# Optimization experiments

Hardware: AMD Instinct MI355X
Metric: run time of the kernel (lower is better)

## Reference

```python
import jax, jax.numpy as jnp
import numpy as np

B, S, D, H, L = 128, 256, 128, 4, 2
N = S - 1            # tree nodes (complete binary tree, depths 0..7)
MAX_DEPTH = 7
NEG = -1e9
EPS = 1e-6


def _binary_tree_topology():
    n = np.arange(N)
    parent = np.where(n > 0, (n - 1) // 2, 0).astype(np.int32)   # parent(0) dummy
    depth = np.floor(np.log2(n + 1)).astype(np.int32)            # BFS level
    is_leaf = (2 * n + 1 >= N)
    return parent, depth, is_leaf


def setup_inputs() -> dict:
    key = jax.random.key(0)
    ks = jax.random.split(key, 6)
    p_np, d_np, l_np = _binary_tree_topology()
    parent = jnp.broadcast_to(jnp.asarray(p_np), (B, N))
    depth = jnp.broadcast_to(jnp.asarray(d_np), (B, N))
    is_leaf = jnp.broadcast_to(jnp.asarray(l_np), (B, N))
    x = jax.random.normal(ks[0], (B, S, D), jnp.float32)
    mask = jnp.zeros((B, 1, 1, S), jnp.float32)  # full trees -> no padding
    sc = 1.0 / np.sqrt(D)
    Wq = jax.random.normal(ks[1], (L, D, D), jnp.float32) * sc
    Wk = jax.random.normal(ks[2], (L, D, D), jnp.float32) * sc
    Wv = jax.random.normal(ks[3], (L, D, D), jnp.float32) * sc
    Wo = jax.random.normal(ks[4], (L, D, D), jnp.float32) * sc
    bq = jnp.zeros((L, D)); bk = jnp.zeros((L, D)); bv = jnp.zeros((L, D)); bo = jnp.zeros((L, D))
    g1 = jnp.ones((L, D)); b1 = jnp.zeros((L, D))
    g2 = jnp.ones((L, D)); b2 = jnp.zeros((L, D))
    return dict(x=x, mask=mask, parent=parent, depth=depth, is_leaf=is_leaf,
                Wq=Wq, bq=bq, Wk=Wk, bk=bk, Wv=Wv, bv=bv, Wo=Wo, bo=bo,
                g1=g1, b1=b1, g2=g2, b2=b2)


def _layernorm(x, g, b):
    mu = jnp.mean(x, axis=-1, keepdims=True)
    var = jnp.mean(jnp.square(x - mu), axis=-1, keepdims=True)
    return g * (x - mu) * jax.lax.rsqrt(var + EPS) + b


def _tree_agg(x, parent, depth, is_leaf):
    """Vectorized bottom-up tree aggregation (agg='sum': tanh(sum children)).
    Seq positions map to tree nodes in BFS order; last position passes through."""
    e = x[:, :N]                                            # [B, N, D]
    seg = (parent + (jnp.arange(B) * N)[:, None]).reshape(-1)  # flat parent ids
    for d in range(MAX_DEPTH, 0, -1):                       # deepest level -> root
        contrib = jnp.where((depth == d)[..., None], e, 0.0)
        agg = jax.ops.segment_sum(contrib.reshape(B * N, D), seg,
                                  num_segments=B * N).reshape(B, N, D)
        upd = ((depth == d - 1) & (~is_leaf))[..., None]    # internal nodes at d-1
        e = jnp.where(upd, jnp.tanh(agg), e)
    return jnp.concatenate([e, x[:, N:]], axis=1)


def reference(x, mask, parent, depth, is_leaf,
              Wq, bq, Wk, bk, Wv, bv, Wo, bo, g1, b1, g2, b2):
    Dh = D // H
    scale = 1.0 / jnp.sqrt(jnp.float32(Dh))
    losses = []
    weights = None
    for l in range(L):
        q = (jnp.einsum('bsd,de->bse', x, Wq[l]) + bq[l]).reshape(B, S, H, Dh).transpose(0, 2, 1, 3)
        k = (jnp.einsum('bsd,de->bse', x, Wk[l]) + bk[l]).reshape(B, S, H, Dh).transpose(0, 2, 1, 3)
        v = (jnp.einsum('bsd,de->bse', x, Wv[l]) + bv[l]).reshape(B, S, H, Dh).transpose(0, 2, 1, 3)
        logits = jnp.einsum('bhqd,bhkd->bhqk', q, k) * scale + mask * NEG
        attn = jax.nn.softmax(logits, axis=-1)              # [B, H, S, S]
        ctx = jnp.einsum('bhqk,bhkd->bhqd', attn, v).transpose(0, 2, 1, 3).reshape(B, S, D)
        att_out = jnp.einsum('bsd,de->bse', ctx, Wo[l]) + bo[l]
        out1 = _layernorm(x + att_out, g1[l], b1[l])
        tab = _tree_agg(out1, parent, depth, is_leaf)       # dropout: eval -> identity
        x = _layernorm(out1 + tab, g2[l], b2[l])
        weights = attn[:, :, -1, :]
        losses.append(jnp.sum(jnp.abs(weights)))
    total_l1 = jnp.sum(jnp.stack(losses))
    return x, total_l1, weights
```

## Files before the change

kernel.cpp:

```cpp
#include <hip/hip_runtime.h>
#include <math.h>

typedef __bf16 bf16x8 __attribute__((ext_vector_type(8)));
typedef __bf16 bf16x4 __attribute__((ext_vector_type(4)));
typedef __bf16 bf16x2 __attribute__((ext_vector_type(2)));
typedef float f32x4 __attribute__((ext_vector_type(4)));

namespace {
constexpr int kB = 128, kS = 256, kD = 128, kH = 4;
constexpr float kEps = 1e-6f;
constexpr float kScale = 0.17677669529663687f;
constexpr float kNeg = -1000000000.0f;
constexpr float kLog2e = 1.4426950408889634f;
constexpr size_t kSZ = (size_t)kB * kS * kD;
}

__device__ __forceinline__ void glds16(const void* g, void* l) {
    __builtin_amdgcn_global_load_lds(
        (const __attribute__((address_space(1))) unsigned int*)g,
        (__attribute__((address_space(3))) unsigned int*)l, 16, 0, 0);
}

__global__ __launch_bounds__(256) void wtrans(
    const float* __restrict__ Wq, const float* __restrict__ Wk,
    const float* __restrict__ Wv, const float* __restrict__ Wo,
    __bf16* __restrict__ Wt)
{
    const int mtx = blockIdx.x & 3, l = blockIdx.x >> 2;
    const float* W = (mtx == 0 ? Wq : mtx == 1 ? Wk : mtx == 2 ? Wv : Wo) +
                     (size_t)l * kD * kD;
    __bf16* o = Wt + (size_t)blockIdx.x * kD * kD;
    for (int idx = threadIdx.x; idx < kD * kD; idx += 256) {
        const int k = idx >> 7, n = idx & 127;
        const int lo = n & 15, ni = n >> 4;
        const int j = k & 7, tt = k >> 3, g = tt & 3, ks = tt >> 2;
        o[((ni * 4 + ks) * 64 + g * 16 + lo) * 8 + j] = (__bf16)W[idx];
    }
}

template <int WEIGHTS, bool F32X>
__global__ __launch_bounds__(512) void mega_attn(
    const void* __restrict__ xsrc, const __bf16* __restrict__ Wp,
    const float* __restrict__ bq, const float* __restrict__ bk,
    const float* __restrict__ bv, const float* __restrict__ bo,
    const float* __restrict__ mask, const float* __restrict__ gamma,
    const float* __restrict__ beta, __bf16* __restrict__ O1,
    float* __restrict__ wout, float* __restrict__ l1out)
{
    __shared__ __bf16 Xs[256 * 128];
    __shared__ __bf16 Kls[256 * 32];
    __shared__ __bf16 Vt[32][276];
    __shared__ __bf16 Pl[8][16 * 64];
    __shared__ __bf16 Qs[8][16 * 32];
    __shared__ __bf16 Ctx[128 * 128];
    __shared__ float mb[256];

    const int t = threadIdx.x;
    const int w = t >> 6, l = t & 63, lo = l & 15, g = l >> 4;
    const int b = blockIdx.x & 127, strip = blockIdx.x >> 7;
    const int q0 = strip * 128 + w * 16;
    const int tk0 = w * 32;
    const int kswz = (lo ^ (lo >> 2)) & 3;

    const __bf16* Wqp = Wp;
    const __bf16* Wkp = Wp + 16384;
    const __bf16* Wvp = Wp + 2 * 16384;
    const __bf16* Wop = Wp + 3 * 16384;

    if constexpr (F32X) {
#pragma unroll
        for (int p = 0; p < 8; ++p) {
            const int ci = p * 512 + t;
            const int row = ci >> 4, c = ci & 15;
            const float* src = (const float*)xsrc +
                               ((size_t)b * 256 + row) * 128 + c * 8;
            const float4 a0 = *(const float4*)src;
            const float4 a1 = *(const float4*)(src + 4);
            bf16x8 o;
            o[0] = (__bf16)a0.x; o[1] = (__bf16)a0.y; o[2] = (__bf16)a0.z; o[3] = (__bf16)a0.w;
            o[4] = (__bf16)a1.x; o[5] = (__bf16)a1.y; o[6] = (__bf16)a1.z; o[7] = (__bf16)a1.w;
            *(bf16x8*)&Xs[row * 128 + ((c ^ (row & 7)) << 3)] = o;
        }
    } else {
#pragma unroll
        for (int it = 0; it < 8; ++it)
            glds16((const __bf16*)xsrc + (size_t)b * 32768 + (it * 8 + w) * 512 + l * 8,
                   &Xs[(it * 8 + w) * 512]);
    }
    if (t < 256) mb[t] = mask[b * 256 + t] * (kNeg * kLog2e);
    if (WEIGHTS && blockIdx.x == 0 && t == 0) l1out[0] = 1024.0f;
    __syncthreads();

    auto wfrag = [&](const __bf16* W, int ni, int ks) {
        return *(const bf16x8*)(W + (((ni * 4 + ks) * 64 + l) << 3));
    };
    auto xfrag = [&](int row, int ks) {
        return *(const bf16x8*)&Xs[row * 128 + (((g + 4 * ks) ^ (row & 7)) << 3)];
    };

    bf16x8 xa[2][4], xq[4];
#pragma unroll
    for (int ks = 0; ks < 4; ++ks) {
        xa[0][ks] = xfrag(tk0 + lo, ks);
        xa[1][ks] = xfrag(tk0 + 16 + lo, ks);
        xq[ks] = xfrag(q0 + lo, ks);
    }

    f32x4 kacc[2][2], vacc[2][2], qacc[2];

    auto produce_compute = [&](int h) {
#pragma unroll
        for (int i = 0; i < 2; ++i)
#pragma unroll
            for (int j2 = 0; j2 < 2; ++j2) {
                kacc[i][j2] = f32x4{0.f, 0.f, 0.f, 0.f};
                vacc[i][j2] = f32x4{0.f, 0.f, 0.f, 0.f};
            }
        qacc[0] = f32x4{0.f, 0.f, 0.f, 0.f};
        qacc[1] = f32x4{0.f, 0.f, 0.f, 0.f};
#pragma unroll
        for (int ks = 0; ks < 4; ++ks) {
            const bf16x8 wk0 = wfrag(Wkp, 2 * h, ks);
            const bf16x8 wk1 = wfrag(Wkp, 2 * h + 1, ks);
            const bf16x8 wv0 = wfrag(Wvp, 2 * h, ks);
            const bf16x8 wv1 = wfrag(Wvp, 2 * h + 1, ks);
            kacc[0][0] = __builtin_amdgcn_mfma_f32_16x16x32_bf16(wk0, xa[0][ks], kacc[0][0], 0, 0, 0);
            kacc[0][1] = __builtin_amdgcn_mfma_f32_16x16x32_bf16(wk0, xa[1][ks], kacc[0][1], 0, 0, 0);
            kacc[1][0] = __builtin_amdgcn_mfma_f32_16x16x32_bf16(wk1, xa[0][ks], kacc[1][0], 0, 0, 0);
            kacc[1][1] = __builtin_amdgcn_mfma_f32_16x16x32_bf16(wk1, xa[1][ks], kacc[1][1], 0, 0, 0);
            vacc[0][0] = __builtin_amdgcn_mfma_f32_16x16x32_bf16(xa[0][ks], wv0, vacc[0][0], 0, 0, 0);
            vacc[1][0] = __builtin_amdgcn_mfma_f32_16x16x32_bf16(xa[1][ks], wv0, vacc[1][0], 0, 0, 0);
            vacc[0][1] = __builtin_amdgcn_mfma_f32_16x16x32_bf16(xa[0][ks], wv1, vacc[0][1], 0, 0, 0);
            vacc[1][1] = __builtin_amdgcn_mfma_f32_16x16x32_bf16(xa[1][ks], wv1, vacc[1][1], 0, 0, 0);
            qacc[0] = __builtin_amdgcn_mfma_f32_16x16x32_bf16(xq[ks], wfrag(Wqp, 2 * h, ks), qacc[0], 0, 0, 0);
            qacc[1] = __builtin_amdgcn_mfma_f32_16x16x32_bf16(xq[ks], wfrag(Wqp, 2 * h + 1, ks), qacc[1], 0, 0, 0);
        }
    };

    auto produce_write = [&](int h) {
#pragma unroll
        for (int dm = 0; dm < 2; ++dm) {
            const f32x4 bkv = *(const f32x4*)(bk + h * 32 + dm * 16 + 4 * g);
            const int pos = ((dm * 2 + (g >> 1)) ^ kswz) << 3;
            const int sub = (4 * g) & 7;
#pragma unroll
            for (int tj = 0; tj < 2; ++tj) {
                bf16x4 kv;
#pragma unroll
                for (int r = 0; r < 4; ++r) kv[r] = (__bf16)(kacc[dm][tj][r] + bkv[r]);
                const int key = tk0 + tj * 16 + lo;
                *(bf16x4*)&Kls[key * 32 + pos + sub] = kv;
            }
        }
#pragma unroll
        for (int nj = 0; nj < 2; ++nj) {
            const float bvv = bv[h * 32 + nj * 16 + lo];
#pragma unroll
            for (int mi = 0; mi < 2; ++mi) {
                bf16x4 vv4;
#pragma unroll
                for (int r = 0; r < 4; ++r) vv4[r] = (__bf16)(vacc[mi][nj][r] + bvv);
                *(bf16x4*)&Vt[nj * 16 + lo][tk0 + mi * 16 + 4 * g] = vv4;
            }
        }
#pragma unroll
        for (int nj = 0; nj < 2; ++nj) {
            const float bqv = bq[h * 32 + nj * 16 + lo];
#pragma unroll
            for (int r = 0; r < 4; ++r)
                Qs[w][(4 * g + r) * 32 + nj * 16 + lo] = (__bf16)(qacc[nj][r] + bqv);
        }
    };

    produce_compute(0);
    produce_write(0);
    __syncthreads();

#pragma unroll
    for (int h = 0; h < 4; ++h) {
        const bf16x8 qf = *(const bf16x8*)&Qs[w][lo * 32 + g * 8];
        f32x4 s[16];
        __builtin_amdgcn_s_setprio(1);
#pragma unroll
        for (int f = 0; f < 16; ++f) {
            const bf16x8 kf =
                *(const bf16x8*)&Kls[(f * 16 + lo) * 32 + ((g ^ kswz) << 3)];
            s[f] = __builtin_amdgcn_mfma_f32_16x16x32_bf16(
                kf, qf, f32x4{0.f, 0.f, 0.f, 0.f}, 0, 0, 0);
        }
        __builtin_amdgcn_s_setprio(0);

        float ls = 0.f;
#pragma unroll
        for (int f = 0; f < 16; ++f) {
            const f32x4 mk = *(const f32x4*)&mb[f * 16 + g * 4];
#pragma unroll
            for (int r = 0; r < 4; ++r) {
                const float p = __builtin_amdgcn_exp2f(
                    s[f][r] * (kScale * kLog2e) + mk[r]);
                s[f][r] = p;
                ls += p;
            }
        }
        ls += __shfl_xor(ls, 16, 64);
        ls += __shfl_xor(ls, 32, 64);

        if constexpr (WEIGHTS) {
            if (strip == 1 && w == 7 && lo == 15) {
                const float inv = 1.f / ls;
                float* wrow = wout + ((size_t)b * 4 + h) * 256;
#pragma unroll
                for (int f = 0; f < 16; ++f)
#pragma unroll
                    for (int r = 0; r < 4; ++r)
                        wrow[f * 16 + g * 4 + r] = s[f][r] * inv;
            }
        }

        f32x4 o[2] = {f32x4{0.f, 0.f, 0.f, 0.f}, f32x4{0.f, 0.f, 0.f, 0.f}};
#pragma unroll
        for (int qt = 0; qt < 4; ++qt) {
#pragma unroll
            for (int fl = 0; fl < 4; ++fl) {
                const int ff = qt * 4 + fl;
#pragma unroll
                for (int pr = 0; pr < 2; ++pr) {
                    bf16x2 pk;
                    pk[0] = (__bf16)s[ff][2 * pr];
                    pk[1] = (__bf16)s[ff][2 * pr + 1];
                    const int e = fl * 16 + 4 * g + 2 * pr;
                    const int addr =
                        lo * 64 + ((((e >> 3) ^ (lo & 7)) << 3) | (e & 7));
                    *(bf16x2*)&Pl[w][addr] = pk;
                }
            }
            __builtin_amdgcn_s_setprio(1);
#pragma unroll
            for (int ksl = 0; ksl < 2; ++ksl) {
                const int cc = ksl * 4 + g;
                const bf16x8 pa =
                    *(const bf16x8*)&Pl[w][lo * 64 + ((cc ^ (lo & 7)) << 3)];
#pragma unroll
                for (int nf = 0; nf < 2; ++nf) {
                    const bf16x8 bvv =
                        *(const bf16x8*)&Vt[nf * 16 + lo][(qt * 2 + ksl) * 32 + g * 8];
                    o[nf] = __builtin_amdgcn_mfma_f32_16x16x32_bf16(pa, bvv, o[nf], 0, 0, 0);
                }
            }
            __builtin_amdgcn_s_setprio(0);
        }

        if (h < 3) produce_compute(h + 1);

#pragma unroll
        for (int r = 0; r < 4; ++r) {
            const float inv = 1.f / __shfl(ls, 4 * g + r, 64);
            const int crow = w * 16 + g * 4 + r;
#pragma unroll
            for (int nf = 0; nf < 2; ++nf) {
                const int col = h * 32 + nf * 16 + lo;
                const int chunk = (col >> 3) ^ (crow & 7);
                Ctx[crow * 128 + (chunk << 3) + (col & 7)] = (__bf16)(o[nf][r] * inv);
            }
        }
        if (h < 3) {
            __syncthreads();
            produce_write(h + 1);
            __syncthreads();
        }
    }

    const size_t m0 = (size_t)b * 256 + strip * 128;
    f32x4 acc[8];
#pragma unroll
    for (int ni = 0; ni < 8; ++ni) acc[ni] = f32x4{0.f, 0.f, 0.f, 0.f};

    const int arow = w * 16 + lo;
#pragma unroll
    for (int ks = 0; ks < 4; ++ks) {
        const bf16x8 av =
            *(const bf16x8*)&Ctx[arow * 128 + (((g + 4 * ks) ^ (arow & 7)) << 3)];
#pragma unroll
        for (int ni = 0; ni < 8; ++ni)
            acc[ni] = __builtin_amdgcn_mfma_f32_16x16x32_bf16(
                av, wfrag(Wop, ni, ks), acc[ni], 0, 0, 0);
    }

    float bcol[8], ga[8], be[8];
#pragma unroll
    for (int ni = 0; ni < 8; ++ni) {
        bcol[ni] = bo[ni * 16 + lo];
        ga[ni] = gamma[ni * 16 + lo];
        be[ni] = beta[ni * 16 + lo];
    }

    float vv[4][8];
    float s[4] = {0, 0, 0, 0}, s2[4] = {0, 0, 0, 0};
#pragma unroll
    for (int r = 0; r < 4; ++r) {
        const int local = strip * 128 + w * 16 + g * 4 + r;
#pragma unroll
        for (int ni = 0; ni < 8; ++ni) {
            const int col = ni * 16 + lo;
            const int chunk = (col >> 3) ^ (local & 7);
            const float rv = (float)Xs[local * 128 + (chunk << 3) + (col & 7)];
            const float x = acc[ni][r] + bcol[ni] + rv;
            vv[r][ni] = x; s[r] += x; s2[r] += x * x;
        }
    }
#pragma unroll
    for (int r = 0; r < 4; ++r)
#pragma unroll
        for (int o = 1; o < 16; o <<= 1) {
            s[r] += __shfl_xor(s[r], o, 64);
            s2[r] += __shfl_xor(s2[r], o, 64);
        }
#pragma unroll
    for (int r = 0; r < 4; ++r) {
        const float mu = s[r] * (1.f / 128.f);
        const float var = s2[r] * (1.f / 128.f) - mu * mu;
        const float rs = rsqrtf(var + kEps);
        const size_t mm = m0 + w * 16 + g * 4 + r;
#pragma unroll
        for (int ni = 0; ni < 8; ++ni)
            O1[mm * 128 + ni * 16 + lo] =
                (__bf16)(ga[ni] * (vv[r][ni] - mu) * rs + be[ni]);
    }
}

__global__ __launch_bounds__(1024) void tree_ln(
    const __bf16* __restrict__ o1, const float* __restrict__ gamma,
    const float* __restrict__ beta, float* __restrict__ xo,
    __bf16* __restrict__ xb, int wf32, int wbf16)
{
    __shared__ float e[127 * 132];
    const int isleaf = blockIdx.x >> 7;
    const int b = blockIdx.x & 127;
    const int t = threadIdx.x;
    const __bf16* ob = o1 + (size_t)b * 256 * 128;
    const int wv = t >> 6, lane = t & 63;
    const float2 gv = *(const float2*)(gamma + lane * 2);
    const float2 bb = *(const float2*)(beta + lane * 2);
    const int c = lane * 2;

    auto ln_store = [&](int row, float y0, float y1) {
        float s = y0 + y1, s2 = y0 * y0 + y1 * y1;
#pragma unroll
        for (int o = 1; o < 64; o <<= 1) {
            s += __shfl_xor(s, o, 64);
            s2 += __shfl_xor(s2, o, 64);
        }
        const float mu = s * (1.f / 128.f);
        const float var = s2 * (1.f / 128.f) - mu * mu;
        const float rs = rsqrtf(var + kEps);
        const float r0 = gv.x * (y0 - mu) * rs + bb.x;
        const float r1 = gv.y * (y1 - mu) * rs + bb.y;
        const size_t rowoff = ((size_t)b * 256 + row) * 128;
        if (wf32) {
            float2 o2; o2.x = r0; o2.y = r1;
            *(float2*)(xo + rowoff + c) = o2;
        }
        if (wbf16) {
            const int chunk = (c >> 3) ^ (row & 7);
            bf16x2 ob2; ob2[0] = (__bf16)r0; ob2[1] = (__bf16)r1;
            *(bf16x2*)(xb + rowoff + chunk * 8 + (c & 7)) = ob2;
        }
    };

    if (isleaf) {
        for (int row = 128 + wv; row < 256; row += 16) {
            const bf16x2 v = *(const bf16x2*)(ob + (size_t)row * 128 + c);
            ln_store(row, 2.f * (float)v[0], 2.f * (float)v[1]);
        }
        return;
    }

    {
        const int p = 63 + (t >> 4);
        const int cg = (t & 15) * 8;
        const bf16x8 c1 = *(const bf16x8*)(ob + (size_t)(2 * p + 1) * 128 + cg);
        const bf16x8 c2 = *(const bf16x8*)(ob + (size_t)(2 * p + 2) * 128 + cg);
        f32x4 r0, r1;
#pragma unroll
        for (int i = 0; i < 4; ++i)
            r0[i] = tanhf((float)c1[i] + (float)c2[i]);
#pragma unroll
        for (int i = 0; i < 4; ++i)
            r1[i] = tanhf((float)c1[4 + i] + (float)c2[4 + i]);
        *(f32x4*)&e[p * 132 + cg] = r0;
        *(f32x4*)&e[p * 132 + cg + 4] = r1;
    }
    __syncthreads();

    {
        const int col = wv * 8 + (lane & 7);
        const int nsub = lane >> 3;
        for (int lvl = 5; lvl >= 0; --lvl) {
            const int p0 = (1 << lvl) - 1;
            const int cnt = 1 << lvl;
            for (int base = 0; base < cnt; base += 8) {
                const int p = p0 + base + nsub;
                if (base + nsub < cnt) {
                    e[p * 132 + col] =
                        tanhf(e[(2 * p + 1) * 132 + col] + e[(2 * p + 2) * 132 + col]);
                }
            }
        }
    }
    __syncthreads();

    for (int row = wv; row < 128; row += 16) {
        const bf16x2 v = *(const bf16x2*)(ob + (size_t)row * 128 + c);
        float y0, y1;
        if (row < 127) {
            y0 = (float)v[0] + e[row * 132 + c];
            y1 = (float)v[1] + e[row * 132 + c + 1];
        } else {
            y0 = 2.f * (float)v[0];
            y1 = 2.f * (float)v[1];
        }
        ln_store(row, y0, y1);
    }
}

extern "C" void kernel_launch(void* const* d_in, const int* in_sizes, int n_in,
                              void* d_out, int out_size, void* d_ws, size_t ws_size,
                              hipStream_t stream)
{
    (void)in_sizes; (void)n_in; (void)out_size; (void)ws_size;

    const float* x_in = (const float*)d_in[0];
    const float* mask = (const float*)d_in[1];
    const float* Wq = (const float*)d_in[5];
    const float* bq = (const float*)d_in[6];
    const float* Wk = (const float*)d_in[7];
    const float* bk = (const float*)d_in[8];
    const float* Wv = (const float*)d_in[9];
    const float* bv = (const float*)d_in[10];
    const float* Wo = (const float*)d_in[11];
    const float* bo = (const float*)d_in[12];
    const float* g1 = (const float*)d_in[13];
    const float* b1 = (const float*)d_in[14];
    const float* g2 = (const float*)d_in[15];
    const float* b2 = (const float*)d_in[16];

    float* out_x = (float*)d_out;
    float* out_l1 = out_x + kSZ;
    float* out_w = out_l1 + 1;

    char* wsb = (char*)d_ws;
    __bf16* O1 = (__bf16*)wsb;
    __bf16* xb = (__bf16*)(wsb + kSZ * 2);
    __bf16* Wt = (__bf16*)(wsb + 2 * kSZ * 2);

    wtrans<<<8, 256, 0, stream>>>(Wq, Wk, Wv, Wo, Wt);

    mega_attn<0, true><<<256, 512, 0, stream>>>(x_in, Wt, bq, bk, bv, bo,
                                                mask, g1, b1, O1,
                                                nullptr, nullptr);
    tree_ln<<<256, 1024, 0, stream>>>(O1, g2, b2, nullptr, xb, 0, 1);

    mega_attn<1, false><<<256, 512, 0, stream>>>(xb, Wt + 4 * 16384,
                                                 bq + kD, bk + kD, bv + kD, bo + kD,
                                                 mask, g1 + kD, b1 + kD, O1,
                                                 out_w, out_l1);
    tree_ln<<<256, 1024, 0, stream>>>(O1, g2 + kD, b2 + kD, out_x, nullptr, 1, 0);
}
```

Measured before the change: 95.01 us.

## Fuse all layers into one persistent kernel with software grid barriers

Replaces the five separate launches (weight transpose, two attention kernels, two tree/LayerNorm kernels) with a single 256-block persistent kernel that uses atomic-counter grid barriers between phases. The leaf-row LayerNorm is folded into the attention epilogue of strip 1, so the tree phase only runs on strip-0 blocks and is remapped to 512 threads. The aim is to remove kernel launch gaps and a redundant pass over leaf rows. In exchange it needs all 256 blocks co-resident to avoid deadlock, adds a memset plus spin-wait barriers, and leaves half the blocks idle during the tree phases.

```diff
diff --git a/kernel.cpp b/kernel.cpp
--- a/kernel.cpp
+++ b/kernel.cpp
@@ -7,13 +7,23 @@
 typedef float f32x4 __attribute__((ext_vector_type(4)));
 
 namespace {
-constexpr int kB = 128, kS = 256, kD = 128, kH = 4;
+constexpr int kD = 128;
 constexpr float kEps = 1e-6f;
 constexpr float kScale = 0.17677669529663687f;
 constexpr float kNeg = -1000000000.0f;
 constexpr float kLog2e = 1.4426950408889634f;
-constexpr size_t kSZ = (size_t)kB * kS * kD;
-}
+constexpr size_t kSZ = (size_t)128 * 256 * 128;
+}
+
+struct SMem {
+    __bf16 Xs[256 * 128];
+    __bf16 Kls[256 * 32];
+    __bf16 Vt[32][276];
+    __bf16 Pl[8][1024];
+    __bf16 Qs[8][512];
+    __bf16 Ctx[128 * 128];
+    float mb[256];
+};
 
 __device__ __forceinline__ void glds16(const void* g, void* l) {
     __builtin_amdgcn_global_load_lds(
@@ -21,40 +31,26 @@
         (__attribute__((address_space(3))) unsigned int*)l, 16, 0, 0);
 }
 
-__global__ __launch_bounds__(256) void wtrans(
-    const float* __restrict__ Wq, const float* __restrict__ Wk,
-    const float* __restrict__ Wv, const float* __restrict__ Wo,
-    __bf16* __restrict__ Wt)
+__device__ __forceinline__ void gridbar(int* cnt, int nblk) {
+    __syncthreads();
+    if (threadIdx.x == 0) {
+        __threadfence();
+        atomicAdd(cnt, 1);
+        while (__hip_atomic_load(cnt, __ATOMIC_ACQUIRE,
+                                 __HIP_MEMORY_SCOPE_AGENT) < nblk)
+            __builtin_amdgcn_s_sleep(2);
+        __threadfence();
+    }
+    __syncthreads();
+}
+
+template <int WEIGHTS, bool STAGE, int LEAF2>
+__device__ void mega_phase(
+    SMem& sm, const void* xsrc, const __bf16* Wp,
+    const float* bq, const float* bk, const float* bv, const float* bo,
+    const float* g1, const float* b1, const float* g2, const float* b2,
+    __bf16* O1, float* wout, float* l1out, float* xo2, __bf16* xb2)
 {
-    const int mtx = blockIdx.x & 3, l = blockIdx.x >> 2;
-    const float* W = (mtx == 0 ? Wq : mtx == 1 ? Wk : mtx == 2 ? Wv : Wo) +
-                     (size_t)l * kD * kD;
-    __bf16* o = Wt + (size_t)blockIdx.x * kD * kD;
-    for (int idx = threadIdx.x; idx < kD * kD; idx += 256) {
-        const int k = idx >> 7, n = idx & 127;
-        const int lo = n & 15, ni = n >> 4;
-        const int j = k & 7, tt = k >> 3, g = tt & 3, ks = tt >> 2;
-        o[((ni * 4 + ks) * 64 + g * 16 + lo) * 8 + j] = (__bf16)W[idx];
-    }
-}
-
-template <int WEIGHTS, bool F32X>
-__global__ __launch_bounds__(512) void mega_attn(
-    const void* __restrict__ xsrc, const __bf16* __restrict__ Wp,
-    const float* __restrict__ bq, const float* __restrict__ bk,
-    const float* __restrict__ bv, const float* __restrict__ bo,
-    const float* __restrict__ mask, const float* __restrict__ gamma,
-    const float* __restrict__ beta, __bf16* __restrict__ O1,
-    float* __restrict__ wout, float* __restrict__ l1out)
-{
-    __shared__ __bf16 Xs[256 * 128];
-    __shared__ __bf16 Kls[256 * 32];
-    __shared__ __bf16 Vt[32][276];
-    __shared__ __bf16 Pl[8][16 * 64];
-    __shared__ __bf16 Qs[8][16 * 32];
-    __shared__ __bf16 Ctx[128 * 128];
-    __shared__ float mb[256];
-
     const int t = threadIdx.x;
     const int w = t >> 6, l = t & 63, lo = l & 15, g = l >> 4;
     const int b = blockIdx.x & 127, strip = blockIdx.x >> 7;
@@ -67,35 +63,20 @@
     const __bf16* Wvp = Wp + 2 * 16384;
     const __bf16* Wop = Wp + 3 * 16384;
 
-    if constexpr (F32X) {
-#pragma unroll
-        for (int p = 0; p < 8; ++p) {
-            const int ci = p * 512 + t;
-            const int row = ci >> 4, c = ci & 15;
-            const float* src = (const float*)xsrc +
-                               ((size_t)b * 256 + row) * 128 + c * 8;
-            const float4 a0 = *(const float4*)src;
-            const float4 a1 = *(const float4*)(src + 4);
-            bf16x8 o;
-            o[0] = (__bf16)a0.x; o[1] = (__bf16)a0.y; o[2] = (__bf16)a0.z; o[3] = (__bf16)a0.w;
-            o[4] = (__bf16)a1.x; o[5] = (__bf16)a1.y; o[6] = (__bf16)a1.z; o[7] = (__bf16)a1.w;
-            *(bf16x8*)&Xs[row * 128 + ((c ^ (row & 7)) << 3)] = o;
-        }
-    } else {
+    if constexpr (STAGE) {
 #pragma unroll
         for (int it = 0; it < 8; ++it)
             glds16((const __bf16*)xsrc + (size_t)b * 32768 + (it * 8 + w) * 512 + l * 8,
-                   &Xs[(it * 8 + w) * 512]);
-    }
-    if (t < 256) mb[t] = mask[b * 256 + t] * (kNeg * kLog2e);
+                   &sm.Xs[(it * 8 + w) * 512]);
+        __syncthreads();
+    }
     if (WEIGHTS && blockIdx.x == 0 && t == 0) l1out[0] = 1024.0f;
-    __syncthreads();
 
     auto wfrag = [&](const __bf16* W, int ni, int ks) {
         return *(const bf16x8*)(W + (((ni * 4 + ks) * 64 + l) << 3));
     };
     auto xfrag = [&](int row, int ks) {
-        return *(const bf16x8*)&Xs[row * 128 + (((g + 4 * ks) ^ (row & 7)) << 3)];
+        return *(const bf16x8*)&sm.Xs[row * 128 + (((g + 4 * ks) ^ (row & 7)) << 3)];
     };
 
     bf16x8 xa[2][4], xq[4];
@@ -149,7 +130,7 @@
 #pragma unroll
                 for (int r = 0; r < 4; ++r) kv[r] = (__bf16)(kacc[dm][tj][r] + bkv[r]);
                 const int key = tk0 + tj * 16 + lo;
-                *(bf16x4*)&Kls[key * 32 + pos + sub] = kv;
+                *(bf16x4*)&sm.Kls[key * 32 + pos + sub] = kv;
             }
         }
 #pragma unroll
@@ -160,7 +141,7 @@
                 bf16x4 vv4;
 #pragma unroll
                 for (int r = 0; r < 4; ++r) vv4[r] = (__bf16)(vacc[mi][nj][r] + bvv);
-                *(bf16x4*)&Vt[nj * 16 + lo][tk0 + mi * 16 + 4 * g] = vv4;
+                *(bf16x4*)&sm.Vt[nj * 16 + lo][tk0 + mi * 16 + 4 * g] = vv4;
             }
         }
 #pragma unroll
@@ -168,7 +149,7 @@
             const float bqv = bq[h * 32 + nj * 16 + lo];
 #pragma unroll
             for (int r = 0; r < 4; ++r)
-                Qs[w][(4 * g + r) * 32 + nj * 16 + lo] = (__bf16)(qacc[nj][r] + bqv);
+                sm.Qs[w][(4 * g + r) * 32 + nj * 16 + lo] = (__bf16)(qacc[nj][r] + bqv);
         }
     };
 
@@ -178,13 +159,13 @@
 
 #pragma unroll
     for (int h = 0; h < 4; ++h) {
-        const bf16x8 qf = *(const bf16x8*)&Qs[w][lo * 32 + g * 8];
+        const bf16x8 qf = *(const bf16x8*)&sm.Qs[w][lo * 32 + g * 8];
         f32x4 s[16];
         __builtin_amdgcn_s_setprio(1);
 #pragma unroll
         for (int f = 0; f < 16; ++f) {
             const bf16x8 kf =
-                *(const bf16x8*)&Kls[(f * 16 + lo) * 32 + ((g ^ kswz) << 3)];
+                *(const bf16x8*)&sm.Kls[(f * 16 + lo) * 32 + ((g ^ kswz) << 3)];
             s[f] = __builtin_amdgcn_mfma_f32_16x16x32_bf16(
                 kf, qf, f32x4{0.f, 0.f, 0.f, 0.f}, 0, 0, 0);
         }
@@ -193,7 +174,7 @@
         float ls = 0.f;
 #pragma unroll
         for (int f = 0; f < 16; ++f) {
-            const f32x4 mk = *(const f32x4*)&mb[f * 16 + g * 4];
+            const f32x4 mk = *(const f32x4*)&sm.mb[f * 16 + g * 4];
 #pragma unroll
             for (int r = 0; r < 4; ++r) {
                 const float p = __builtin_amdgcn_exp2f(
@@ -231,7 +212,7 @@
                     const int e = fl * 16 + 4 * g + 2 * pr;
                     const int addr =
                         lo * 64 + ((((e >> 3) ^ (lo & 7)) << 3) | (e & 7));
-                    *(bf16x2*)&Pl[w][addr] = pk;
+                    *(bf16x2*)&sm.Pl[w][addr] = pk;
                 }
             }
             __builtin_amdgcn_s_setprio(1);
@@ -239,11 +220,11 @@
             for (int ksl = 0; ksl < 2; ++ksl) {
                 const int cc = ksl * 4 + g;
                 const bf16x8 pa =
-                    *(const bf16x8*)&Pl[w][lo * 64 + ((cc ^ (lo & 7)) << 3)];
+                    *(const bf16x8*)&sm.Pl[w][lo * 64 + ((cc ^ (lo & 7)) << 3)];
 #pragma unroll
                 for (int nf = 0; nf < 2; ++nf) {
                     const bf16x8 bvv =
-                        *(const bf16x8*)&Vt[nf * 16 + lo][(qt * 2 + ksl) * 32 + g * 8];
+                        *(const bf16x8*)&sm.Vt[nf * 16 + lo][(qt * 2 + ksl) * 32 + g * 8];
                     o[nf] = __builtin_amdgcn_mfma_f32_16x16x32_bf16(pa, bvv, o[nf], 0, 0, 0);
                 }
             }
@@ -260,7 +241,7 @@
             for (int nf = 0; nf < 2; ++nf) {
                 const int col = h * 32 + nf * 16 + lo;
                 const int chunk = (col >> 3) ^ (crow & 7);
-                Ctx[crow * 128 + (chunk << 3) + (col & 7)] = (__bf16)(o[nf][r] * inv);
+                sm.Ctx[crow * 128 + (chunk << 3) + (col & 7)] = (__bf16)(o[nf][r] * inv);
             }
         }
         if (h < 3) {
@@ -279,19 +260,26 @@
 #pragma unroll
     for (int ks = 0; ks < 4; ++ks) {
         const bf16x8 av =
-            *(const bf16x8*)&Ctx[arow * 128 + (((g + 4 * ks) ^ (arow & 7)) << 3)];
+            *(const bf16x8*)&sm.Ctx[arow * 128 + (((g + 4 * ks) ^ (arow & 7)) << 3)];
 #pragma unroll
         for (int ni = 0; ni < 8; ++ni)
             acc[ni] = __builtin_amdgcn_mfma_f32_16x16x32_bf16(
                 av, wfrag(Wop, ni, ks), acc[ni], 0, 0, 0);
     }
 
-    float bcol[8], ga[8], be[8];
+    float bcol[8], ga[8], be[8], g2a[8], b2a[8];
 #pragma unroll
     for (int ni = 0; ni < 8; ++ni) {
         bcol[ni] = bo[ni * 16 + lo];
-        ga[ni] = gamma[ni * 16 + lo];
-        be[ni] = beta[ni * 16 + lo];
+        ga[ni] = g1[ni * 16 + lo];
+        be[ni] = b1[ni * 16 + lo];
+    }
+    if (LEAF2 && strip == 1) {
+#pragma unroll
+        for (int ni = 0; ni < 8; ++ni) {
+            g2a[ni] = g2[ni * 16 + lo];
+            b2a[ni] = b2[ni * 16 + lo];
+        }
     }
 
     float vv[4][8];
@@ -303,7 +291,7 @@
         for (int ni = 0; ni < 8; ++ni) {
             const int col = ni * 16 + lo;
             const int chunk = (col >> 3) ^ (local & 7);
-            const float rv = (float)Xs[local * 128 + (chunk << 3) + (col & 7)];
+            const float rv = (float)sm.Xs[local * 128 + (chunk << 3) + (col & 7)];
             const float x = acc[ni][r] + bcol[ni] + rv;
             vv[r][ni] = x; s[r] += x; s2[r] += x * x;
         }
@@ -321,29 +309,96 @@
         const float var = s2[r] * (1.f / 128.f) - mu * mu;
         const float rs = rsqrtf(var + kEps);
         const size_t mm = m0 + w * 16 + g * 4 + r;
-#pragma unroll
-        for (int ni = 0; ni < 8; ++ni)
-            O1[mm * 128 + ni * 16 + lo] =
-                (__bf16)(ga[ni] * (vv[r][ni] - mu) * rs + be[ni]);
-    }
-}
-
-__global__ __launch_bounds__(1024) void tree_ln(
-    const __bf16* __restrict__ o1, const float* __restrict__ gamma,
-    const float* __restrict__ beta, float* __restrict__ xo,
-    __bf16* __restrict__ xb, int wf32, int wbf16)
+        float yv[8];
+        float ys = 0.f, ys2 = 0.f;
+#pragma unroll
+        for (int ni = 0; ni < 8; ++ni) {
+            const __bf16 ov = (__bf16)(ga[ni] * (vv[r][ni] - mu) * rs + be[ni]);
+            O1[mm * 128 + ni * 16 + lo] = ov;
+            if (LEAF2 && strip == 1) {
+                const float y = 2.f * (float)ov;
+                yv[ni] = y; ys += y; ys2 += y * y;
+            }
+        }
+        if (LEAF2 && strip == 1) {
+#pragma unroll
+            for (int o = 1; o < 16; o <<= 1) {
+                ys += __shfl_xor(ys, o, 64);
+                ys2 += __shfl_xor(ys2, o, 64);
+            }
+            const float mu2 = ys * (1.f / 128.f);
+            const float var2 = ys2 * (1.f / 128.f) - mu2 * mu2;
+            const float rs2 = rsqrtf(var2 + kEps);
+#pragma unroll
+            for (int ni = 0; ni < 8; ++ni) {
+                const float val = g2a[ni] * (yv[ni] - mu2) * rs2 + b2a[ni];
+                const int col = ni * 16 + lo;
+                if constexpr (LEAF2 == 1) {
+                    const int chunk = (col >> 3) ^ ((int)mm & 7);
+                    xb2[mm * 128 + chunk * 8 + (col & 7)] = (__bf16)val;
+                } else if constexpr (LEAF2 == 2) {
+                    xo2[mm * 128 + col] = val;
+                }
+            }
+        }
+    }
+}
+
+__device__ void tree_phase0(
+    SMem& sm, const __bf16* O1, const float* gamma, const float* beta,
+    float* xo, __bf16* xb, int wf32, int wbf16, int b)
 {
-    __shared__ float e[127 * 132];
-    const int isleaf = blockIdx.x >> 7;
-    const int b = blockIdx.x & 127;
+    float* e = (float*)sm.Xs;
     const int t = threadIdx.x;
-    const __bf16* ob = o1 + (size_t)b * 256 * 128;
     const int wv = t >> 6, lane = t & 63;
+    const __bf16* ob = O1 + (size_t)b * 32768;
     const float2 gv = *(const float2*)(gamma + lane * 2);
     const float2 bb = *(const float2*)(beta + lane * 2);
     const int c = lane * 2;
 
-    auto ln_store = [&](int row, float y0, float y1) {
+#pragma unroll
+    for (int it = 0; it < 2; ++it) {
+        const int q = it * 512 + t;
+        const int p = 63 + (q >> 4);
+        const int cg = (q & 15) * 8;
+        const bf16x8 c1 = *(const bf16x8*)(ob + (size_t)(2 * p + 1) * 128 + cg);
+        const bf16x8 c2 = *(const bf16x8*)(ob + (size_t)(2 * p + 2) * 128 + cg);
+        f32x4 r0, r1;
+#pragma unroll
+        for (int i = 0; i < 4; ++i) r0[i] = tanhf((float)c1[i] + (float)c2[i]);
+#pragma unroll
+        for (int i = 0; i < 4; ++i) r1[i] = tanhf((float)c1[4 + i] + (float)c2[4 + i]);
+        *(f32x4*)&e[p * 128 + cg] = r0;
+        *(f32x4*)&e[p * 128 + cg + 4] = r1;
+    }
+    __syncthreads();
+
+    {
+        const int col = wv * 16 + (lane & 15);
+        const int nsub = lane >> 4;
+        for (int lvl = 5; lvl >= 0; --lvl) {
+            const int p0 = (1 << lvl) - 1;
+            const int cntn = 1 << lvl;
+            for (int base = 0; base < cntn; base += 4) {
+                const int p = p0 + base + nsub;
+                if (base + nsub < cntn)
+                    e[p * 128 + col] =
+                        tanhf(e[(2 * p + 1) * 128 + col] + e[(2 * p + 2) * 128 + col]);
+            }
+        }
+    }
+    __syncthreads();
+
+    for (int row = wv; row < 128; row += 8) {
+        const bf16x2 v = *(const bf16x2*)(ob + (size_t)row * 128 + c);
+        float y0, y1;
+        if (row < 127) {
+            y0 = (float)v[0] + e[row * 128 + c];
+            y1 = (float)v[1] + e[row * 128 + c + 1];
+        } else {
+            y0 = 2.f * (float)v[0];
+            y1 = 2.f * (float)v[1];
+        }
         float s = y0 + y1, s2 = y0 * y0 + y1 * y1;
 #pragma unroll
         for (int o = 1; o < 64; o <<= 1) {
@@ -365,62 +420,68 @@
             bf16x2 ob2; ob2[0] = (__bf16)r0; ob2[1] = (__bf16)r1;
             *(bf16x2*)(xb + rowoff + chunk * 8 + (c & 7)) = ob2;
         }
-    };
-
-    if (isleaf) {
-        for (int row = 128 + wv; row < 256; row += 16) {
-            const bf16x2 v = *(const bf16x2*)(ob + (size_t)row * 128 + c);
-            ln_store(row, 2.f * (float)v[0], 2.f * (float)v[1]);
-        }
-        return;
-    }
-
+    }
+}
+
+__global__ __launch_bounds__(512) void fused_net(
+    const float* __restrict__ x_in, const float* __restrict__ mask,
+    const float* __restrict__ Wq, const float* __restrict__ Wk,
+    const float* __restrict__ Wv, const float* __restrict__ Wo,
+    const float* __restrict__ bq, const float* __restrict__ bk,
+    const float* __restrict__ bv, const float* __restrict__ bo,
+    const float* __restrict__ g1, const float* __restrict__ b1,
+    const float* __restrict__ g2, const float* __restrict__ b2,
+    __bf16* Wt, __bf16* O1, __bf16* xb,
+    float* out_x, float* out_w, float* out_l1, int* cnt)
+{
+    __shared__ SMem sm;
+    const int t = threadIdx.x;
+    const int b = blockIdx.x & 127;
+    const int strip = blockIdx.x >> 7;
+
+#pragma unroll
+    for (int p = 0; p < 8; ++p) {
+        const int ci = p * 512 + t;
+        const int row = ci >> 4, cc = ci & 15;
+        const float* src = x_in + ((size_t)b * 256 + row) * 128 + cc * 8;
+        const float4 a0 = *(const float4*)src;
+        const float4 a1 = *(const float4*)(src + 4);
+        bf16x8 o;
+        o[0] = (__bf16)a0.x; o[1] = (__bf16)a0.y; o[2] = (__bf16)a0.z; o[3] = (__bf16)a0.w;
+        o[4] = (__bf16)a1.x; o[5] = (__bf16)a1.y; o[6] = (__bf16)a1.z; o[7] = (__bf16)a1.w;
+        *(bf16x8*)&sm.Xs[row * 128 + ((cc ^ (row & 7)) << 3)] = o;
+    }
     {
-        const int p = 63 + (t >> 4);
-        const int cg = (t & 15) * 8;
-        const bf16x8 c1 = *(const bf16x8*)(ob + (size_t)(2 * p + 1) * 128 + cg);
-        const bf16x8 c2 = *(const bf16x8*)(ob + (size_t)(2 * p + 2) * 128 + cg);
-        f32x4 r0, r1;
-#pragma unroll
-        for (int i = 0; i < 4; ++i)
-            r0[i] = tanhf((float)c1[i] + (float)c2[i]);
-#pragma unroll
-        for (int i = 0; i < 4; ++i)
-            r1[i] = tanhf((float)c1[4 + i] + (float)c2[4 + i]);
-        *(f32x4*)&e[p * 132 + cg] = r0;
-        *(f32x4*)&e[p * 132 + cg + 4] = r1;
-    }
-    __syncthreads();
-
-    {
-        const int col = wv * 8 + (lane & 7);
-        const int nsub = lane >> 3;
-        for (int lvl = 5; lvl >= 0; --lvl) {
-            const int p0 = (1 << lvl) - 1;
-            const int cnt = 1 << lvl;
-            for (int base = 0; base < cnt; base += 8) {
-                const int p = p0 + base + nsub;
-                if (base + nsub < cnt) {
-                    e[p * 132 + col] =
-                        tanhf(e[(2 * p + 1) * 132 + col] + e[(2 * p + 2) * 132 + col]);
-                }
-            }
-        }
-    }
-    __syncthreads();
-
-    for (int row = wv; row < 128; row += 16) {
-        const bf16x2 v = *(const bf16x2*)(ob + (size_t)row * 128 + c);
-        float y0, y1;
-        if (row < 127) {
-            y0 = (float)v[0] + e[row * 132 + c];
-            y1 = (float)v[1] + e[row * 132 + c + 1];
-        } else {
-            y0 = 2.f * (float)v[0];
-            y1 = 2.f * (float)v[1];
-        }
-        ln_store(row, y0, y1);
-    }
+        const int idx = blockIdx.x * 512 + t;
+        const int m = idx >> 14;
+        const int rest = idx & 16383;
+        const int k = rest >> 7, n = rest & 127;
+        const float* srcs[4] = {Wq, Wk, Wv, Wo};
+        const float v = srcs[m & 3][(size_t)(m >> 2) * 16384 + rest];
+        const int lo2 = n & 15, ni = n >> 4;
+        const int j = k & 7, tt = k >> 3, gg = tt & 3, ks = tt >> 2;
+        Wt[(size_t)m * 16384 + ((ni * 4 + ks) * 64 + gg * 16 + lo2) * 8 + j] = (__bf16)v;
+    }
+    if (t < 256) sm.mb[t] = mask[b * 256 + t] * (kNeg * kLog2e);
+
+    gridbar(cnt + 0, 256);
+
+    mega_phase<0, false, 1>(sm, nullptr, Wt, bq, bk, bv, bo, g1, b1, g2, b2,
+                            O1, nullptr, nullptr, nullptr, xb);
+    gridbar(cnt + 1, 256);
+
+    if (strip == 0)
+        tree_phase0(sm, O1, g2, b2, nullptr, xb, 0, 1, b);
+    gridbar(cnt + 2, 256);
+
+    mega_phase<1, true, 2>(sm, xb, Wt + 4 * 16384,
+                           bq + kD, bk + kD, bv + kD, bo + kD,
+                           g1 + kD, b1 + kD, g2 + kD, b2 + kD,
+                           O1, out_w, out_l1, out_x, nullptr);
+    gridbar(cnt + 3, 256);
+
+    if (strip == 0)
+        tree_phase0(sm, O1, g2 + kD, b2 + kD, out_x, nullptr, 1, 0, b);
 }
 
 extern "C" void kernel_launch(void* const* d_in, const int* in_sizes, int n_in,
@@ -452,17 +513,10 @@
     __bf16* O1 = (__bf16*)wsb;
     __bf16* xb = (__bf16*)(wsb + kSZ * 2);
     __bf16* Wt = (__bf16*)(wsb + 2 * kSZ * 2);
-
-    wtrans<<<8, 256, 0, stream>>>(Wq, Wk, Wv, Wo, Wt);
-
-    mega_attn<0, true><<<256, 512, 0, stream>>>(x_in, Wt, bq, bk, bv, bo,
-                                                mask, g1, b1, O1,
-                                                nullptr, nullptr);
-    tree_ln<<<256, 1024, 0, stream>>>(O1, g2, b2, nullptr, xb, 0, 1);
-
-    mega_attn<1, false><<<256, 512, 0, stream>>>(xb, Wt + 4 * 16384,
-                                                 bq + kD, bk + kD, bv + kD, bo + kD,
-                                                 mask, g1 + kD, b1 + kD, O1,
-                                                 out_w, out_l1);
-    tree_ln<<<256, 1024, 0, stream>>>(O1, g2 + kD, b2 + kD, out_x, nullptr, 1, 0);
-}
+    int* cnt = (int*)(wsb + 2 * kSZ * 2 + 8 * 16384 * 2);
+
+    hipMemsetAsync(cnt, 0, 4 * sizeof(int), stream);
+    fused_net<<<256, 512, 0, stream>>>(x_in, mask, Wq, Wk, Wv, Wo,
+                                       bq, bk, bv, bo, g1, b1, g2, b2,
+                                       Wt, O1, xb, out_x, out_w, out_l1, cnt);
+}
```

After: 273.3 us. +187.7%, slower.
